# Optimization experiments

Measured on AMD Instinct MI355X. Metric: run time of the kernel, lower is better.

The kernel has to match this reference:

```python
import jax, jax.numpy as jnp
import numpy as np

B, I, H, R = 8192, 1024, 1024, 16  # batch, input_size, hidden_size, subspace_size


def setup_inputs() -> dict:
    key = jax.random.key(0)
    ks = jax.random.split(key, 11)
    s_in = 1.0 / np.sqrt(I)
    s_h = 1.0 / np.sqrt(H)
    return {
        "x": jax.random.normal(ks[0], (B, I), jnp.float32),
        "h0": jax.random.normal(ks[1], (B, H), jnp.float32),
        "c0": jax.random.normal(ks[2], (B, H), jnp.float32),
        # stacked per-gate params, gate order: [i, f, g, o]
        "W_i": jax.random.normal(ks[3], (4, H, I), jnp.float32) * s_in,
        "W_h": jax.random.normal(ks[4], (4, H, H), jnp.float32) * s_h,
        "b_i": jnp.zeros((4, H), jnp.float32),
        "b_h": jnp.zeros((4, H), jnp.float32),
        "A_i": jax.random.normal(ks[5], (4, R, I), jnp.float32),
        "B_i": jax.random.normal(ks[6], (4, H, R), jnp.float32) * 0.01,
        "A_h": jax.random.normal(ks[7], (4, R, H), jnp.float32),
        "B_h": jax.random.normal(ks[8], (4, H, R), jnp.float32) * 0.01,
    }


def reference(x, h0, c0, W_i, W_h, b_i, b_h, A_i, B_i, A_h, B_h):
    # Pre-activation for all 4 gates at once: [B, 4, H]
    pre = (
        jnp.einsum("bi,ghi->bgh", x, W_i)
        + jnp.einsum("bk,ghk->bgh", h0, W_h)
        + b_i[None, :, :]
        + b_h[None, :, :]
        # LoRA: x @ (B@A).T == (x @ A.T) @ B.T, done in factored (efficient) form
        + jnp.einsum("bgr,ghr->bgh", jnp.einsum("bi,gri->bgr", x, A_i), B_i)
        + jnp.einsum("bgr,ghr->bgh", jnp.einsum("bk,grk->bgr", h0, A_h), B_h)
    )
    i_t = jax.nn.sigmoid(pre[:, 0])
    f_t = jax.nn.sigmoid(pre[:, 1])
    g_t = jnp.tanh(pre[:, 2])
    o_t = jax.nn.sigmoid(pre[:, 3])
    c_t = f_t * c0 + i_t * g_t
    h_t = o_t * jnp.tanh(c_t)
    return (h_t, c_t)
```

## Files before the change

### kernel.cpp

```cpp
#include <hip/hip_runtime.h>
#include <hip/hip_bf16.h>
#include <cstdint>

#define B_  8192
#define I_  1024
#define H_  1024
#define R_  16
#define K_  2048
#define N_  4096

typedef __attribute__((ext_vector_type(4))) float f32x4;
typedef __attribute__((ext_vector_type(8))) __bf16 bf16x8;
typedef __attribute__((ext_vector_type(8))) unsigned short u16x8;
typedef __attribute__((ext_vector_type(4))) unsigned short u16x4;
typedef unsigned short u16;

__device__ __forceinline__ u16 f2bf(float f) {
  union { float f; unsigned u; } v; v.f = f;
  unsigned u = v.u;
  return (u16)((u + 0x7fffu + ((u >> 16) & 1u)) >> 16);
}

__device__ __forceinline__ float sigmoidf_(float x) {
  return 1.0f / (1.0f + __expf(-x));
}
__device__ __forceinline__ float tanhf_(float x) {
  return 1.0f - 2.0f / (__expf(2.0f * x) + 1.0f);
}

__global__ __launch_bounds__(256) void prep_all(
    const float* __restrict__ x, const float* __restrict__ h0,
    const float* __restrict__ W_i, const float* __restrict__ W_h,
    const float* __restrict__ b_i, const float* __restrict__ b_h,
    const float* __restrict__ A_i, const float* __restrict__ Bi,
    const float* __restrict__ A_h, const float* __restrict__ Bh,
    u16* __restrict__ Xc, u16* __restrict__ Wc, float* __restrict__ bc) {
  const int bid = blockIdx.x;
  const int tid = threadIdx.x;
  if (bid < 8192) {
    int idx = bid * 256 + tid;
    int e = idx << 3;
    int b = e >> 11;
    int k = e & (K_ - 1);
    const float* src = (k < I_) ? (x + ((size_t)b << 10) + k)
                                : (h0 + ((size_t)b << 10) + (k - I_));
    const f32x4 v0 = *(const f32x4*)src;
    const f32x4 v1 = *(const f32x4*)(src + 4);
    u16x8 o;
    o[0] = f2bf(v0[0]); o[1] = f2bf(v0[1]); o[2] = f2bf(v0[2]); o[3] = f2bf(v0[3]);
    o[4] = f2bf(v1[0]); o[5] = f2bf(v1[1]); o[6] = f2bf(v1[2]); o[7] = f2bf(v1[3]);
    *(u16x8*)(Xc + (size_t)e) = o;
  } else {
    const int gh = bid - 8192;
    const int g = gh >> 10, h = gh & (H_ - 1);
    float bi[R_], bh[R_];
#pragma unroll
    for (int r = 0; r < R_; ++r) {
      bi[r] = Bi[((size_t)(g * H_ + h) << 4) + r];
      bh[r] = Bh[((size_t)(g * H_ + h) << 4) + r];
    }
    u16* dst = Wc + (size_t)(h * 4 + g) * K_;
    const float* wi = W_i + ((size_t)(g * H_ + h) << 10);
    const float* wh = W_h + ((size_t)(g * H_ + h) << 10);
    const int k4 = tid * 4;
    f32x4 accI = *(const f32x4*)&wi[k4];
    f32x4 accH = *(const f32x4*)&wh[k4];
#pragma unroll
    for (int r = 0; r < R_; ++r) {
      const f32x4 ai = *(const f32x4*)&A_i[((size_t)(g * R_ + r) << 10) + k4];
      const f32x4 ah = *(const f32x4*)&A_h[((size_t)(g * R_ + r) << 10) + k4];
      accI += bi[r] * ai;
      accH += bh[r] * ah;
    }
    u16x4 oi, oh;
#pragma unroll
    for (int j = 0; j < 4; ++j) { oi[j] = f2bf(accI[j]); oh[j] = f2bf(accH[j]); }
    *(u16x4*)(dst + k4) = oi;
    *(u16x4*)(dst + I_ + k4) = oh;
    if (tid == 0) bc[h * 4 + g] = b_i[g * H_ + h] + b_h[g * H_ + h];
  }
}

#define BM 256
#define BN 256
#define BK 64
#define NT (K_ / BK)

#define GLOAD_LDS16(gp, lp)                                                        \
  __builtin_amdgcn_global_load_lds(                                                \
      (const __attribute__((address_space(1))) void*)(gp),                         \
      (__attribute__((address_space(3))) void*)(lp), 16, 0, 0)

#define BAR()                                                                      \
  do { asm volatile("" ::: "memory"); __builtin_amdgcn_s_barrier();                \
       asm volatile("" ::: "memory"); } while (0)

#define BARL()                                                                     \
  do { asm volatile("s_waitcnt lgkmcnt(0)" ::: "memory");                          \
       __builtin_amdgcn_s_barrier(); asm volatile("" ::: "memory"); } while (0)

#define WAITV0() asm volatile("s_waitcnt vmcnt(0)" ::: "memory")
#define WAITV4() asm volatile("s_waitcnt vmcnt(4)" ::: "memory")
#define WAITV6() asm volatile("s_waitcnt vmcnt(6)" ::: "memory")

#define AH(HI, SL) ((u16*)(lds_raw + ((HI) * 2 + (SL)) * 16384))
#define BH(HI, SL) ((u16*)(lds_raw + 65536 + ((HI) * 2 + (SL)) * 16384))

#define STAGE_H(GBASE, HALF, K0N, REGION)                                          \
  _Pragma("unroll")                                                                \
  for (int r_ = 0; r_ < 2; ++r_) {                                                 \
    int chunk_ = r_ * 512 + tid;                                                   \
    int rl_ = chunk_ >> 3, cp_ = chunk_ & 7;                                       \
    int cc_ = cp_ ^ (rl_ & 7);                                                     \
    GLOAD_LDS16((GBASE) + (size_t)((HALF) * 128 + rl_) * K_ + (K0N) + cc_ * 8,     \
                (char*)(REGION) + chunk_ * 16);                                    \
  }

#define READ_Av(REGION, AV)                                                        \
  _Pragma("unroll")                                                                \
  for (int mi_ = 0; mi_ < 4; ++mi_) {                                              \
    _Pragma("unroll")                                                              \
    for (int kk_ = 0; kk_ < 2; ++kk_) {                                            \
      const int rl_ = wave_m + mi_ * 16 + lr;                                      \
      AV[mi_][kk_] = *(const bf16x8*)&(REGION)[rl_ * 64 +                          \
          (((kk_ * 4 + lk) ^ (rl_ & 7)) << 3)];                                    \
    }                                                                              \
  }

#define READ_B(REGION, BV)                                                         \
  _Pragma("unroll")                                                                \
  for (int nj_ = 0; nj_ < 2; ++nj_) {                                              \
    _Pragma("unroll")                                                              \
    for (int kk_ = 0; kk_ < 2; ++kk_) {                                            \
      const int rl_ = wave_n + nj_ * 16 + lr;                                      \
      BV[nj_][kk_] = *(const bf16x8*)&(REGION)[rl_ * 64 +                          \
          (((kk_ * 4 + lk) ^ (rl_ & 7)) << 3)];                                    \
    }                                                                              \
  }

#define MMA(MH, NH, BV, AV)                                                        \
  do {                                                                             \
    __builtin_amdgcn_s_setprio(1);                                                 \
    _Pragma("unroll")                                                              \
    for (int mi_ = 0; mi_ < 4; ++mi_)                                              \
      _Pragma("unroll")                                                            \
      for (int nj_ = 0; nj_ < 2; ++nj_)                                            \
        _Pragma("unroll")                                                          \
        for (int kk_ = 0; kk_ < 2; ++kk_)                                          \
          acc[(MH) * 4 + mi_][(NH) * 2 + nj_] =                                    \
              __builtin_amdgcn_mfma_f32_16x16x32_bf16(                             \
                  AV[mi_][kk_], BV[nj_][kk_],                                      \
                  acc[(MH) * 4 + mi_][(NH) * 2 + nj_], 0, 0, 0);                   \
    __builtin_amdgcn_s_setprio(0);                                                 \
  } while (0)

#define KTILE(CB, NB, T)                                                           \
  do {                                                                             \
    const int k1_ = ((T) + 1 < NT) ? ((T) + 1) * BK : 0;                           \
    const int k2_ = ((T) + 2 < NT) ? ((T) + 2) * BK : 0;                           \
    BAR();                                                                         \
    STAGE_H(Ag, 1, k1_, AH(1, NB));                                                \
    MMA(0, 0, bv0, av0);                                                           \
    READ_Av(AH(1, CB), av1);                                                       \
    BAR();                                                                         \
    STAGE_H(Bg, 0, k2_, BH(0, CB));                                                \
    MMA(1, 0, bv0, av1);                                                           \
    READ_B(BH(1, CB), bv1);                                                        \
    BAR();                                                                         \
    STAGE_H(Ag, 0, k2_, AH(0, CB));                                                \
    MMA(1, 1, bv1, av1);                                                           \
    WAITV4();                                                                      \
    BAR();                                                                         \
    STAGE_H(Bg, 1, k2_, BH(1, CB));                                                \
    MMA(0, 1, bv1, av0);                                                           \
    READ_Av(AH(0, NB), av0);                                                       \
    READ_B(BH(0, NB), bv0);                                                        \
  } while (0)

__global__ __launch_bounds__(512, 2) void lstm_gemm(
    const u16* __restrict__ Xc, const u16* __restrict__ Wc,
    const float* __restrict__ bc, const float* __restrict__ c0,
    float* __restrict__ out) {
  __shared__ __align__(16) char lds_raw[131072];

  const int tid = threadIdx.x;
  const int wave = tid >> 6, lane = tid & 63;
  const int lr = lane & 15, lk = lane >> 4;

  const int flat = blockIdx.y * gridDim.x + blockIdx.x;
  const int swz = (flat & 7) * 64 + (flat >> 3);
  const int bm = swz >> 4, bn = swz & 15;
  const int m0 = bm * BM, n0 = bn * BN;

  const int wave_m = (wave >> 2) * 64;
  const int wave_n = (wave & 3) * 32;

  f32x4 acc[8][4] = {};
  bf16x8 av0[4][2], av1[4][2], bv0[2][2], bv1[2][2];

  const u16* Ag = Xc + (size_t)m0 * K_;
  const u16* Bg = Wc + (size_t)n0 * K_;

  STAGE_H(Ag, 0, 0, AH(0, 0));
  STAGE_H(Bg, 0, 0, BH(0, 0));
  STAGE_H(Ag, 1, 0, AH(1, 0));
  STAGE_H(Bg, 1, 0, BH(1, 0));
  STAGE_H(Bg, 0, BK, BH(0, 1));
  STAGE_H(Ag, 0, BK, AH(0, 1));
  STAGE_H(Bg, 1, BK, BH(1, 1));
  WAITV6();
  BAR();
  READ_Av(AH(0, 0), av0);
  READ_B(BH(0, 0), bv0);

#pragma unroll 1
  for (int tt = 0; tt < NT; tt += 2) {
    KTILE(0, 1, tt);
    KTILE(1, 0, tt + 1);
  }

  WAITV0();
  float* lE = (float*)lds_raw;
  float biasv[4];
#pragma unroll
  for (int an = 0; an < 4; ++an)
    biasv[an] = bc[n0 + (an >> 1) * 128 + wave_n + (an & 1) * 16 + lr];

#pragma unroll
  for (int half = 0; half < 2; ++half) {
    BARL();
#pragma unroll
    for (int mi = 0; mi < 4; ++mi)
#pragma unroll
      for (int an = 0; an < 4; ++an)
#pragma unroll
        for (int j = 0; j < 4; ++j) {
          const int row = wave_m + mi * 16 + lk * 4 + j;
          const int col = (an >> 1) * 128 + wave_n + (an & 1) * 16 + lr;
          const int colx = col ^ ((((row & 3) ^ ((row >> 2) & 3))) << 4);
          lE[row * 256 + colx] = acc[half * 4 + mi][an][j] + biasv[an];
        }
    BARL();
#pragma unroll
    for (int jj = 0; jj < 4; ++jj) {
      const int item = jj * 512 + tid;
      const int hl4 = item & 15;
      const int rr = item >> 4;
      const int xorv = ((rr & 3) ^ ((rr >> 2) & 3)) << 4;
      const int grow = m0 + half * 128 + rr;
      const int hg = (n0 >> 2) + hl4 * 4;
      const f32x4 c0v = *(const f32x4*)&c0[(size_t)grow * H_ + hg];
      f32x4 htv, ctv;
#pragma unroll
      for (int q = 0; q < 4; ++q) {
        const int colx = (hl4 * 16 + q * 4) ^ xorv;
        const f32x4 pre = *(const f32x4*)&lE[rr * 256 + colx];
        float ig = sigmoidf_(pre[0]);
        float fg = sigmoidf_(pre[1]);
        float gg = tanhf_(pre[2]);
        float og = sigmoidf_(pre[3]);
        float ct = fg * c0v[q] + ig * gg;
        htv[q] = og * tanhf_(ct);
        ctv[q] = ct;
      }
      *(f32x4*)&out[(size_t)grow * H_ + hg] = htv;
      *(f32x4*)&out[(size_t)(B_ * H_) + (size_t)grow * H_ + hg] = ctv;
    }
  }
}

extern "C" void kernel_launch(void* const* d_in, const int* in_sizes, int n_in,
                              void* d_out, int out_size, void* d_ws, size_t ws_size,
                              hipStream_t stream) {
  const float* x   = (const float*)d_in[0];
  const float* h0  = (const float*)d_in[1];
  const float* c0  = (const float*)d_in[2];
  const float* W_i = (const float*)d_in[3];
  const float* W_h = (const float*)d_in[4];
  const float* b_i = (const float*)d_in[5];
  const float* b_h = (const float*)d_in[6];
  const float* A_i = (const float*)d_in[7];
  const float* B_i = (const float*)d_in[8];
  const float* A_h = (const float*)d_in[9];
  const float* B_h = (const float*)d_in[10];
  float* out = (float*)d_out;

  char* ws = (char*)d_ws;
  u16*   Xc = (u16*)ws;
  u16*   Wc = (u16*)(ws + ((size_t)32 << 20));
  float* bc = (float*)(ws + ((size_t)48 << 20));

  prep_all<<<dim3(8192 + 4096), dim3(256), 0, stream>>>(
      x, h0, W_i, W_h, b_i, b_h, A_i, B_i, A_h, B_h, Xc, Wc, bc);
  lstm_gemm<<<dim3(N_ / BN, B_ / BM), dim3(512), 0, stream>>>(Xc, Wc, bc, c0, out);
}
```

Measured before the change: 170.5 us.

## Restructure K-tile pipeline into two barrier phases with 32-MFMA blocks

Result: no change. 171.6 us (+0.7%).

```diff
diff --git a/kernel.cpp b/kernel.cpp
--- a/kernel.cpp
+++ b/kernel.cpp
@@ -100,7 +100,7 @@
        __builtin_amdgcn_s_barrier(); asm volatile("" ::: "memory"); } while (0)
 
 #define WAITV0() asm volatile("s_waitcnt vmcnt(0)" ::: "memory")
-#define WAITV4() asm volatile("s_waitcnt vmcnt(4)" ::: "memory")
+#define WAITV2() asm volatile("s_waitcnt vmcnt(2)" ::: "memory")
 #define WAITV6() asm volatile("s_waitcnt vmcnt(6)" ::: "memory")
 
 #define AH(HI, SL) ((u16*)(lds_raw + ((HI) * 2 + (SL)) * 16384))
@@ -138,19 +138,28 @@
     }                                                                              \
   }
 
-#define MMA(MH, NH, BV, AV)                                                        \
+#define MMA32(NH, BV)                                                              \
   do {                                                                             \
     __builtin_amdgcn_s_setprio(1);                                                 \
     _Pragma("unroll")                                                              \
-    for (int mi_ = 0; mi_ < 4; ++mi_)                                              \
+    for (int kk_ = 0; kk_ < 2; ++kk_) {                                            \
       _Pragma("unroll")                                                            \
-      for (int nj_ = 0; nj_ < 2; ++nj_)                                            \
+      for (int mi_ = 0; mi_ < 4; ++mi_)                                            \
         _Pragma("unroll")                                                          \
-        for (int kk_ = 0; kk_ < 2; ++kk_)                                          \
-          acc[(MH) * 4 + mi_][(NH) * 2 + nj_] =                                    \
+        for (int nj_ = 0; nj_ < 2; ++nj_)                                          \
+          acc[mi_][(NH) * 2 + nj_] =                                               \
               __builtin_amdgcn_mfma_f32_16x16x32_bf16(                             \
-                  AV[mi_][kk_], BV[nj_][kk_],                                      \
-                  acc[(MH) * 4 + mi_][(NH) * 2 + nj_], 0, 0, 0);                   \
+                  av0[mi_][kk_], BV[nj_][kk_],                                     \
+                  acc[mi_][(NH) * 2 + nj_], 0, 0, 0);                              \
+      _Pragma("unroll")                                                            \
+      for (int mi_ = 0; mi_ < 4; ++mi_)                                            \
+        _Pragma("unroll")                                                          \
+        for (int nj_ = 0; nj_ < 2; ++nj_)                                          \
+          acc[4 + mi_][(NH) * 2 + nj_] =                                           \
+              __builtin_amdgcn_mfma_f32_16x16x32_bf16(                             \
+                  av1[mi_][kk_], BV[nj_][kk_],                                     \
+                  acc[4 + mi_][(NH) * 2 + nj_], 0, 0, 0);                          \
+    }                                                                              \
     __builtin_amdgcn_s_setprio(0);                                                 \
   } while (0)
 
@@ -158,23 +167,19 @@
   do {                                                                             \
     const int k1_ = ((T) + 1 < NT) ? ((T) + 1) * BK : 0;                           \
     const int k2_ = ((T) + 2 < NT) ? ((T) + 2) * BK : 0;                           \
+    READ_Av(AH(0, CB), av0);                                                       \
+    READ_Av(AH(1, CB), av1);                                                       \
+    READ_B(BH(0, CB), bv);                                                         \
     BAR();                                                                         \
     STAGE_H(Ag, 1, k1_, AH(1, NB));                                                \
-    MMA(0, 0, bv0, av0);                                                           \
-    READ_Av(AH(1, CB), av1);                                                       \
-    BAR();                                                                         \
     STAGE_H(Bg, 0, k2_, BH(0, CB));                                                \
-    MMA(1, 0, bv0, av1);                                                           \
-    READ_B(BH(1, CB), bv1);                                                        \
+    MMA32(0, bv);                                                                  \
+    READ_B(BH(1, CB), bv);                                                         \
+    WAITV2();                                                                      \
     BAR();                                                                         \
     STAGE_H(Ag, 0, k2_, AH(0, CB));                                                \
-    MMA(1, 1, bv1, av1);                                                           \
-    WAITV4();                                                                      \
-    BAR();                                                                         \
     STAGE_H(Bg, 1, k2_, BH(1, CB));                                                \
-    MMA(0, 1, bv1, av0);                                                           \
-    READ_Av(AH(0, NB), av0);                                                       \
-    READ_B(BH(0, NB), bv0);                                                        \
+    MMA32(1, bv);                                                                  \
   } while (0)
 
 __global__ __launch_bounds__(512, 2) void lstm_gemm(
@@ -196,22 +201,20 @@
   const int wave_n = (wave & 3) * 32;
 
   f32x4 acc[8][4] = {};
-  bf16x8 av0[4][2], av1[4][2], bv0[2][2], bv1[2][2];
+  bf16x8 av0[4][2], av1[4][2], bv[2][2];
 
   const u16* Ag = Xc + (size_t)m0 * K_;
   const u16* Bg = Wc + (size_t)n0 * K_;
 
   STAGE_H(Ag, 0, 0, AH(0, 0));
   STAGE_H(Bg, 0, 0, BH(0, 0));
+  STAGE_H(Bg, 1, 0, BH(1, 0));
   STAGE_H(Ag, 1, 0, AH(1, 0));
-  STAGE_H(Bg, 1, 0, BH(1, 0));
   STAGE_H(Bg, 0, BK, BH(0, 1));
   STAGE_H(Ag, 0, BK, AH(0, 1));
   STAGE_H(Bg, 1, BK, BH(1, 1));
   WAITV6();
   BAR();
-  READ_Av(AH(0, 0), av0);
-  READ_B(BH(0, 0), bv0);
 
 #pragma unroll 1
   for (int tt = 0; tt < NT; tt += 2) {
```
